# Kernel optimization log

Hardware: AMD Instinct MI355X
Metric: run time of the kernel (lower is better)

The kernel has to match this reference:

```python
import jax, jax.numpy as jnp
import numpy as np

BN_EPS = 1e-5


def _batchnorm(x, gamma, beta):
    # BatchNorm1d in training mode: per-batch mean and biased variance
    mean = jnp.mean(x, axis=0)
    var = jnp.mean((x - mean) ** 2, axis=0)
    return gamma * (x - mean) / jnp.sqrt(var + BN_EPS) + beta


def setup_inputs() -> dict:
    key = jax.random.key(0)
    ks = jax.random.split(key, 8)
    N, D, H, C = 400000, 192, 192, 8
    inputs = jax.random.normal(ks[0], (N, D), dtype=jnp.float32)
    labels = jax.random.randint(ks[1], (N,), 0, C, dtype=jnp.int64)
    s = 0.05
    return {
        "inputs": inputs,
        "labels": labels,
        "W1": jax.random.normal(ks[2], (D, H), dtype=jnp.float32) * s,
        "b1": jnp.zeros((H,), dtype=jnp.float32),
        "g1": jnp.ones((H,), dtype=jnp.float32),
        "be1": jnp.zeros((H,), dtype=jnp.float32),
        "W2": jax.random.normal(ks[3], (H, H), dtype=jnp.float32) * s,
        "b2": jnp.zeros((H,), dtype=jnp.float32),
        "g2": jnp.ones((H,), dtype=jnp.float32),
        "be2": jnp.zeros((H,), dtype=jnp.float32),
        "W3": jax.random.normal(ks[4], (H, C), dtype=jnp.float32) * s,
        "b3": jnp.zeros((C,), dtype=jnp.float32),
    }


def reference(inputs, labels, W1, b1, g1, be1, W2, b2, g2, be2, W3, b3):
    # The per-unique-label mask/concat loop is equivalent to a stable sort by label
    order = jnp.argsort(labels, stable=True)
    fea = inputs[order]              # [N, D]
    domain_ids = labels[order]       # [N]
    # ReverseLayerF is identity in the forward pass
    h = jax.nn.relu(_batchnorm(fea @ W1 + b1, g1, be1))
    h = jax.nn.relu(_batchnorm(h @ W2 + b2, g2, be2))
    pred = jax.nn.sigmoid(h @ W3 + b3)   # [N, C]
    logp = jax.nn.log_softmax(pred, axis=-1)
    loss = -jnp.mean(jnp.take_along_axis(logp, domain_ids[:, None], axis=1))
    return loss
```

## Files before the change

### kernel.cpp

```cpp
#include <hip/hip_runtime.h>

typedef unsigned char u8;
typedef unsigned short u16;
typedef unsigned int u32;
typedef long long i64;
typedef __attribute__((ext_vector_type(2))) float f32x2;
typedef __attribute__((ext_vector_type(4))) float f32x4;

#define NROWS 400000
#define DIM 192
#define GRPB 64
#define GNBLK (NROWS / GRPB)
#define FRPB 128
#define FNBLK (NROWS / FRPB)
#define SLAB 25
#define RBLK (GNBLK / SLAB)
#define PITCH 208
#define BN_EPS 1e-5f

__device__ __forceinline__ u16 f2b(float f) {
  union { float f; u32 u; } v; v.f = f;
  return (u16)((v.u + 0x7fffu + ((v.u >> 16) & 1u)) >> 16);
}

#if __has_builtin(__builtin_amdgcn_cvt_pk_fp8_f32) && __has_builtin(__builtin_amdgcn_cvt_pk_f32_fp8)
#define HW_FP8 1
#endif

__device__ __forceinline__ u32 enc1_fp8(float f) {
  float a = fabsf(f);
  u32 sg = (__float_as_uint(f) >> 24) & 0x80u;
  a = fminf(a, 448.f);
  u32 em;
  if (a >= 0.015625f) {
    u32 b = __float_as_uint(a);
    b += 0x0007FFFFu + ((b >> 20) & 1u);
    em = ((b >> 20) & 0xFFFu) - 960u;
  } else {
    em = (u32)(int)rintf(a * 512.f);
  }
  return sg | em;
}
__device__ __forceinline__ float dec1_fp8(u32 b) {
  u32 em = b & 0x7Fu;
  float vn = __uint_as_float((em + 960u) << 20);
  float vd = (float)em * 0.001953125f;
  float v = (em >= 8u) ? vn : vd;
  return (b & 0x80u) ? -v : v;
}

__device__ __forceinline__ u32 pack4_fp8(float f0, float f1, float f2, float f3) {
#ifdef HW_FP8
  int w = 0;
  w = __builtin_amdgcn_cvt_pk_fp8_f32(f0, f1, w, false);
  w = __builtin_amdgcn_cvt_pk_fp8_f32(f2, f3, w, true);
  return (u32)w;
#else
  return enc1_fp8(f0) | (enc1_fp8(f1) << 8) | (enc1_fp8(f2) << 16) | (enc1_fp8(f3) << 24);
#endif
}

__device__ __forceinline__ void unpack8_fp8(uint2 p, float (&f)[8]) {
#ifdef HW_FP8
  f32x2 v0 = __builtin_amdgcn_cvt_pk_f32_fp8(p.x, false);
  f32x2 v1 = __builtin_amdgcn_cvt_pk_f32_fp8(p.x, true);
  f32x2 v2 = __builtin_amdgcn_cvt_pk_f32_fp8(p.y, false);
  f32x2 v3 = __builtin_amdgcn_cvt_pk_f32_fp8(p.y, true);
  f[0] = v0[0]; f[1] = v0[1]; f[2] = v1[0]; f[3] = v1[1];
  f[4] = v2[0]; f[5] = v2[1]; f[6] = v3[0]; f[7] = v3[1];
#else
#pragma unroll
  for (int i = 0; i < 4; ++i) f[i] = dec1_fp8((p.x >> (8 * i)) & 0xFFu);
#pragma unroll
  for (int i = 0; i < 4; ++i) f[4 + i] = dec1_fp8((p.y >> (8 * i)) & 0xFFu);
#endif
}

__device__ __forceinline__ i64 u2l(uint2 u) {
  union { uint2 u2; i64 l; } c; c.u2 = u; return c.l;
}

__global__ void prep_w(const float* __restrict__ W1, const float* __restrict__ W2,
                       const float* __restrict__ W3, u8* __restrict__ W1q,
                       u8* __restrict__ W2q, u8* __restrict__ W3q) {
  int idx = blockIdx.x * 256 + threadIdx.x;
  if (idx < DIM * DIM) {
    int h = idx / DIM, d = idx % DIM;
    W1q[idx] = (u8)enc1_fp8(W1[d * DIM + h]);
    W2q[idx] = (u8)enc1_fp8(W2[d * DIM + h]);
  } else if (idx < DIM * DIM + 16 * DIM) {
    int j = idx - DIM * DIM;
    int c = j / DIM, k = j % DIM;
    W3q[j] = (c < 8) ? (u8)enc1_fp8(W3[k * 8 + c]) : (u8)0;
  }
}

template <int LAYER>
__global__ __launch_bounds__(256, 4) void gemm_bn(
    const float* __restrict__ Xf, const u8* __restrict__ Yin8,
    u8* __restrict__ Yout8, const u8* __restrict__ Wq,
    const float* __restrict__ bias, const float* __restrict__ scale_in,
    const float* __restrict__ shift_in, float* __restrict__ partials) {
  __shared__ __align__(16) char smem[GRPB * PITCH];
  const int t = threadIdx.x;
  const int bid = blockIdx.x;
  const size_t row0 = (size_t)bid * GRPB;

  if (LAYER == 1) {
    const float4* Xv = (const float4*)(Xf + row0 * DIM);
#pragma unroll
    for (int j = 0; j < 12; ++j) {
      int e = j * 256 + t;
      int r = e / 48, c4 = e % 48;
      float4 v = Xv[e];
      *(u32*)(smem + r * PITCH + c4 * 4) = pack4_fp8(v.x, v.y, v.z, v.w);
    }
  } else {
    const uint2* Yin2 = (const uint2*)(Yin8 + row0 * DIM);
#pragma unroll
    for (int j = 0; j < 6; ++j) {
      int e = j * 256 + t;
      int r = e / 24, c8 = e % 24;
      int cb8 = c8 * 8;
      uint2 p = Yin2[r * 24 + c8];
      float f[8];
      unpack8_fp8(p, f);
      float4 sc0 = *(const float4*)&scale_in[cb8];
      float4 sc1 = *(const float4*)&scale_in[cb8 + 4];
      float4 sh0 = *(const float4*)&shift_in[cb8];
      float4 sh1 = *(const float4*)&shift_in[cb8 + 4];
      float scv[8] = {sc0.x, sc0.y, sc0.z, sc0.w, sc1.x, sc1.y, sc1.z, sc1.w};
      float shv[8] = {sh0.x, sh0.y, sh0.z, sh0.w, sh1.x, sh1.y, sh1.z, sh1.w};
      float h[8];
#pragma unroll
      for (int i = 0; i < 8; ++i) h[i] = fmaxf(f[i] * scv[i] + shv[i], 0.f);
      uint2 o;
      o.x = pack4_fp8(h[0], h[1], h[2], h[3]);
      o.y = pack4_fp8(h[4], h[5], h[6], h[7]);
      *(uint2*)(smem + r * PITCH + cb8) = o;
    }
  }
  __syncthreads();

  const int lane = t & 63, wv = t >> 6;
  const int cb = wv * 48;
  const int lr = lane & 15;
  const int g = lane >> 4;
  const int kg = g * 8;

  f32x4 acc[4][3];
#pragma unroll
  for (int rt = 0; rt < 4; ++rt)
#pragma unroll
    for (int ct = 0; ct < 3; ++ct) acc[rt][ct] = (f32x4){0.f, 0.f, 0.f, 0.f};

#pragma unroll
  for (int ks = 0; ks < 6; ++ks) {
    const int k0 = ks * 32 + kg;
    i64 b0 = u2l(*(const uint2*)(Wq + (size_t)(cb + lr) * DIM + k0));
    i64 b1 = u2l(*(const uint2*)(Wq + (size_t)(cb + 16 + lr) * DIM + k0));
    i64 b2 = u2l(*(const uint2*)(Wq + (size_t)(cb + 32 + lr) * DIM + k0));
#pragma unroll
    for (int rt = 0; rt < 4; ++rt) {
      i64 a = u2l(*(const uint2*)(smem + (rt * 16 + lr) * PITCH + k0));
      acc[rt][0] = __builtin_amdgcn_mfma_f32_16x16x32_fp8_fp8(b0, a, acc[rt][0], 0, 0, 0);
      acc[rt][1] = __builtin_amdgcn_mfma_f32_16x16x32_fp8_fp8(b1, a, acc[rt][1], 0, 0, 0);
      acc[rt][2] = __builtin_amdgcn_mfma_f32_16x16x32_fp8_fp8(b2, a, acc[rt][2], 0, 0, 0);
    }
  }
  __syncthreads();

  float4 bl[3];
#pragma unroll
  for (int ct = 0; ct < 3; ++ct) bl[ct] = *(const float4*)&bias[cb + ct * 16 + g * 4];
  f32x4 s[3], q[3];
#pragma unroll
  for (int ct = 0; ct < 3; ++ct) { s[ct] = (f32x4){0,0,0,0}; q[ct] = (f32x4){0,0,0,0}; }
  u32* lds32 = (u32*)smem;
#pragma unroll
  for (int rt = 0; rt < 4; ++rt) {
    const int row = rt * 16 + lr;
#pragma unroll
    for (int ct = 0; ct < 3; ++ct) {
      f32x4 v = acc[rt][ct];
      float f0 = v[0] + bl[ct].x, f1 = v[1] + bl[ct].y;
      float f2 = v[2] + bl[ct].z, f3 = v[3] + bl[ct].w;
      s[ct][0] += f0; s[ct][1] += f1; s[ct][2] += f2; s[ct][3] += f3;
      q[ct][0] += f0 * f0; q[ct][1] += f1 * f1; q[ct][2] += f2 * f2; q[ct][3] += f3 * f3;
      lds32[row * 52 + wv * 12 + ct * 4 + g] = pack4_fp8(f0, f1, f2, f3);
    }
  }
  __syncthreads();

  uint4* Yo4 = (uint4*)(Yout8 + row0 * DIM);
#pragma unroll
  for (int u = 0; u < 3; ++u) {
    int idx4 = u * 256 + t;
    int row = idx4 / 12, m = idx4 % 12;
    Yo4[idx4] = *(const uint4*)(smem + row * PITCH + m * 16);
  }

#pragma unroll
  for (int ct = 0; ct < 3; ++ct)
#pragma unroll
    for (int off = 1; off <= 8; off <<= 1)
#pragma unroll
      for (int i = 0; i < 4; ++i) {
        s[ct][i] += __shfl_xor(s[ct][i], off);
        q[ct][i] += __shfl_xor(q[ct][i], off);
      }
  if (lr == 0) {
    size_t base = (size_t)bid * 384 + cb + g * 4;
#pragma unroll
    for (int ct = 0; ct < 3; ++ct) {
      *(f32x4*)&partials[base + ct * 16] = s[ct];
      *(f32x4*)&partials[base + ct * 16 + 192] = q[ct];
    }
  }
}

__global__ __launch_bounds__(384) void bn_reduce1(const float* __restrict__ partials,
                                                  float* __restrict__ out2) {
  const int b = blockIdx.x, t = threadIdx.x;
  const float* p = partials + (size_t)b * SLAB * 384;
  float v = 0.f;
#pragma unroll
  for (int r = 0; r < SLAB; ++r) v += p[r * 384 + t];
  out2[b * 384 + t] = v;
}

__global__ __launch_bounds__(384) void bn_fin2(
    const float* __restrict__ out2, const float* __restrict__ g,
    const float* __restrict__ be, float* __restrict__ scale,
    float* __restrict__ shift, float* accum) {
  __shared__ float tot[384];
  const int t = threadIdx.x;
  float v = 0.f;
  for (int b = 0; b < RBLK; ++b) v += out2[b * 384 + t];
  tot[t] = v;
  __syncthreads();
  if (t < 192) {
    float s = tot[t], q = tot[t + 192];
    float mean = s / (float)NROWS;
    float var = q / (float)NROWS - mean * mean;
    float inv = rsqrtf(var + BN_EPS);
    float sc = g[t] * inv;
    scale[t] = sc;
    shift[t] = be[t] - mean * sc;
  }
  if (t == 0) *accum = 0.f;
}

__global__ __launch_bounds__(256, 4) void final_loss(
    const u8* __restrict__ Y2, const int* __restrict__ labels,
    const float* __restrict__ scale2, const float* __restrict__ shift2,
    const u8* __restrict__ W3q, const float* __restrict__ b3, float* accum) {
  __shared__ __align__(16) char smem[FRPB * PITCH];
  __shared__ __align__(16) float sc2[DIM], sh2[DIM];
  __shared__ float red[4];
  const int t = threadIdx.x;
  const size_t row0 = (size_t)blockIdx.x * FRPB;

  const uint4* Yp4 = (const uint4*)(Y2 + row0 * DIM);
#pragma unroll
  for (int j = 0; j < 6; ++j) {
    int idx4 = j * 256 + t;
    int row = idx4 / 12, m = idx4 % 12;
    *(uint4*)(smem + row * PITCH + m * 16) = Yp4[idx4];
  }
  if (t < 48) ((float4*)sc2)[t] = ((const float4*)scale2)[t];
  else if (t < 96) ((float4*)sh2)[t - 48] = ((const float4*)shift2)[t - 48];
  __syncthreads();

  const int lane = t & 63, wv = t >> 6;
  const int lr = lane & 15, g = lane >> 4, kg = g * 8;
  i64 wf[6];
#pragma unroll
  for (int ks = 0; ks < 6; ++ks)
    wf[ks] = u2l(*(const uint2*)(W3q + lr * DIM + ks * 32 + kg));
  const float b3v = (lr < 8) ? b3[lr] : 0.f;

  float contrib = 0.f;
#pragma unroll
  for (int tl = 0; tl < 2; ++tl) {
    const int rbase = wv * 32 + tl * 16;
    f32x4 acc = (f32x4){0.f, 0.f, 0.f, 0.f};
#pragma unroll
    for (int ks = 0; ks < 6; ++ks) {
      const int k0 = ks * 32 + kg;
      uint2 raw = *(const uint2*)(smem + (rbase + lr) * PITCH + k0);
      float f[8];
      unpack8_fp8(raw, f);
      float4 c0 = *(const float4*)&sc2[k0];
      float4 c1 = *(const float4*)&sc2[k0 + 4];
      float4 d0 = *(const float4*)&sh2[k0];
      float4 d1 = *(const float4*)&sh2[k0 + 4];
      float scv[8] = {c0.x, c0.y, c0.z, c0.w, c1.x, c1.y, c1.z, c1.w};
      float shv[8] = {d0.x, d0.y, d0.z, d0.w, d1.x, d1.y, d1.z, d1.w};
      float h[8];
#pragma unroll
      for (int i = 0; i < 8; ++i) h[i] = fmaxf(f[i] * scv[i] + shv[i], 0.f);
      uint2 af;
      af.x = pack4_fp8(h[0], h[1], h[2], h[3]);
      af.y = pack4_fp8(h[4], h[5], h[6], h[7]);
      acc = __builtin_amdgcn_mfma_f32_16x16x32_fp8_fp8(u2l(af), wf[ks], acc, 0, 0, 0);
    }
#pragma unroll
    for (int i = 0; i < 4; ++i) {
      float p = 1.f / (1.f + __expf(-(acc[i] + b3v)));
      float m = p;
      m = fmaxf(m, __shfl_xor(m, 1));
      m = fmaxf(m, __shfl_xor(m, 2));
      m = fmaxf(m, __shfl_xor(m, 4));
      float e = __expf(p - m);
      e += __shfl_xor(e, 1);
      e += __shfl_xor(e, 2);
      e += __shfl_xor(e, 4);
      int lab = labels[row0 + rbase + g * 4 + i];
      if (lr == lab) contrib += m + __logf(e) - p;
    }
  }
#pragma unroll
  for (int off = 1; off < 64; off <<= 1) contrib += __shfl_xor(contrib, off);
  if (lane == 0) red[wv] = contrib;
  __syncthreads();
  if (t == 0) atomicAdd(accum, red[0] + red[1] + red[2] + red[3]);
}

__global__ void finalize(const float* __restrict__ accum, float* __restrict__ out) {
  if (threadIdx.x == 0) out[0] = accum[0] / (float)NROWS;
}

extern "C" void kernel_launch(void* const* d_in, const int* in_sizes, int n_in,
                              void* d_out, int out_size, void* d_ws, size_t ws_size,
                              hipStream_t stream) {
  const float* inputs = (const float*)d_in[0];
  const int* labels   = (const int*)d_in[1];
  const float* W1  = (const float*)d_in[2];
  const float* b1  = (const float*)d_in[3];
  const float* g1  = (const float*)d_in[4];
  const float* be1 = (const float*)d_in[5];
  const float* W2  = (const float*)d_in[6];
  const float* b2  = (const float*)d_in[7];
  const float* g2  = (const float*)d_in[8];
  const float* be2 = (const float*)d_in[9];
  const float* W3  = (const float*)d_in[10];
  const float* b3  = (const float*)d_in[11];
  float* out = (float*)d_out;

  char* ws = (char*)d_ws;
  u8* W1q       = (u8*)(ws + 0);
  u8* W2q       = (u8*)(ws + 40960);
  u8* W3q       = (u8*)(ws + 81920);
  float* scale1 = (float*)(ws + 98304);
  float* shift1 = (float*)(ws + 99072);
  float* scale2 = (float*)(ws + 99840);
  float* shift2 = (float*)(ws + 100608);
  float* accum  = (float*)(ws + 101376);
  float* out2   = (float*)(ws + 102400);
  float* partials = (float*)(ws + 524288);
  u8* Ybuf      = (u8*)(ws + 16777216);

  prep_w<<<300, 256, 0, stream>>>(W1, W2, W3, W1q, W2q, W3q);
  gemm_bn<1><<<GNBLK, 256, 0, stream>>>(inputs, nullptr, Ybuf, W1q, b1, nullptr, nullptr, partials);
  bn_reduce1<<<RBLK, 384, 0, stream>>>(partials, out2);
  bn_fin2<<<1, 384, 0, stream>>>(out2, g1, be1, scale1, shift1, accum);
  gemm_bn<2><<<GNBLK, 256, 0, stream>>>(nullptr, Ybuf, Ybuf, W2q, b2, scale1, shift1, partials);
  bn_reduce1<<<RBLK, 384, 0, stream>>>(partials, out2);
  bn_fin2<<<1, 384, 0, stream>>>(out2, g2, be2, scale2, shift2, accum);
  final_loss<<<FNBLK, 256, 0, stream>>>(Ybuf, labels, scale2, shift2, W3q, b3, accum);
  finalize<<<1, 64, 0, stream>>>(accum, out);
}
```

Before: 231.8 us.

## Persist GEMM blocks with double-buffered LDS prefetch and drop BN-cancelled biases

Turns gemm_bn and final_loss into persistent kernels over a fixed grid of 768 blocks. Each block loads its weight fragments into registers once, then prefetches the next tile into registers and stages it into a second LDS buffer while the current tile is processed. The b1/b2 bias adds are removed because training-mode batchnorm subtracts the batch mean, which cancels them exactly. Other changes: the LDS pitch shrinks to 200 bytes, the BN apply in final_loss moves into the staging step, and prep_w launches fewer blocks. In exchange, register pressure rises and the occupancy bound drops from 4 to 3 blocks per CU.

```diff
diff --git a/kernel.cpp b/kernel.cpp
--- a/kernel.cpp
+++ b/kernel.cpp
@@ -1,7 +1,6 @@
 #include <hip/hip_runtime.h>
 
 typedef unsigned char u8;
-typedef unsigned short u16;
 typedef unsigned int u32;
 typedef long long i64;
 typedef __attribute__((ext_vector_type(2))) float f32x2;
@@ -10,18 +9,15 @@
 #define NROWS 400000
 #define DIM 192
 #define GRPB 64
-#define GNBLK (NROWS / GRPB)
+#define NTILE (NROWS / GRPB)
+#define GGRID 768
 #define FRPB 128
-#define FNBLK (NROWS / FRPB)
+#define FNTILE (NROWS / FRPB)
+#define FGRID 768
 #define SLAB 25
-#define RBLK (GNBLK / SLAB)
-#define PITCH 208
+#define RBLK (NTILE / SLAB)
+#define PITCH 200
 #define BN_EPS 1e-5f
-
-__device__ __forceinline__ u16 f2b(float f) {
-  union { float f; u32 u; } v; v.f = f;
-  return (u16)((v.u + 0x7fffu + ((v.u >> 16) & 1u)) >> 16);
-}
 
 #if __has_builtin(__builtin_amdgcn_cvt_pk_fp8_f32) && __has_builtin(__builtin_amdgcn_cvt_pk_f32_fp8)
 #define HW_FP8 1
@@ -41,13 +37,6 @@
   }
   return sg | em;
 }
-__device__ __forceinline__ float dec1_fp8(u32 b) {
-  u32 em = b & 0x7Fu;
-  float vn = __uint_as_float((em + 960u) << 20);
-  float vd = (float)em * 0.001953125f;
-  float v = (em >= 8u) ? vn : vd;
-  return (b & 0x80u) ? -v : v;
-}
 
 __device__ __forceinline__ u32 pack4_fp8(float f0, float f1, float f2, float f3) {
 #ifdef HW_FP8
@@ -59,6 +48,16 @@
   return enc1_fp8(f0) | (enc1_fp8(f1) << 8) | (enc1_fp8(f2) << 16) | (enc1_fp8(f3) << 24);
 #endif
 }
+
+#ifndef HW_FP8
+__device__ __forceinline__ float dec1_fp8(u32 b) {
+  u32 em = b & 0x7Fu;
+  float vn = __uint_as_float((em + 960u) << 20);
+  float vd = (float)em * 0.001953125f;
+  float v = (em >= 8u) ? vn : vd;
+  return (b & 0x80u) ? -v : v;
+}
+#endif
 
 __device__ __forceinline__ void unpack8_fp8(uint2 p, float (&f)[8]) {
 #ifdef HW_FP8
@@ -96,127 +95,152 @@
 }
 
 template <int LAYER>
-__global__ __launch_bounds__(256, 4) void gemm_bn(
+__global__ __launch_bounds__(256, 3) void gemm_bn(
     const float* __restrict__ Xf, const u8* __restrict__ Yin8,
     u8* __restrict__ Yout8, const u8* __restrict__ Wq,
-    const float* __restrict__ bias, const float* __restrict__ scale_in,
-    const float* __restrict__ shift_in, float* __restrict__ partials) {
-  __shared__ __align__(16) char smem[GRPB * PITCH];
+    const float* __restrict__ scale_in, const float* __restrict__ shift_in,
+    float* __restrict__ partials) {
+  __shared__ __align__(16) char smem[2][GRPB * PITCH];
   const int t = threadIdx.x;
-  const int bid = blockIdx.x;
-  const size_t row0 = (size_t)bid * GRPB;
-
-  if (LAYER == 1) {
-    const float4* Xv = (const float4*)(Xf + row0 * DIM);
-#pragma unroll
-    for (int j = 0; j < 12; ++j) {
-      int e = j * 256 + t;
-      int r = e / 48, c4 = e % 48;
-      float4 v = Xv[e];
-      *(u32*)(smem + r * PITCH + c4 * 4) = pack4_fp8(v.x, v.y, v.z, v.w);
-    }
-  } else {
-    const uint2* Yin2 = (const uint2*)(Yin8 + row0 * DIM);
-#pragma unroll
-    for (int j = 0; j < 6; ++j) {
-      int e = j * 256 + t;
-      int r = e / 24, c8 = e % 24;
-      int cb8 = c8 * 8;
-      uint2 p = Yin2[r * 24 + c8];
-      float f[8];
-      unpack8_fp8(p, f);
-      float4 sc0 = *(const float4*)&scale_in[cb8];
-      float4 sc1 = *(const float4*)&scale_in[cb8 + 4];
-      float4 sh0 = *(const float4*)&shift_in[cb8];
-      float4 sh1 = *(const float4*)&shift_in[cb8 + 4];
-      float scv[8] = {sc0.x, sc0.y, sc0.z, sc0.w, sc1.x, sc1.y, sc1.z, sc1.w};
-      float shv[8] = {sh0.x, sh0.y, sh0.z, sh0.w, sh1.x, sh1.y, sh1.z, sh1.w};
-      float h[8];
-#pragma unroll
-      for (int i = 0; i < 8; ++i) h[i] = fmaxf(f[i] * scv[i] + shv[i], 0.f);
-      uint2 o;
-      o.x = pack4_fp8(h[0], h[1], h[2], h[3]);
-      o.y = pack4_fp8(h[4], h[5], h[6], h[7]);
-      *(uint2*)(smem + r * PITCH + cb8) = o;
-    }
-  }
-  __syncthreads();
-
   const int lane = t & 63, wv = t >> 6;
-  const int cb = wv * 48;
-  const int lr = lane & 15;
-  const int g = lane >> 4;
-  const int kg = g * 8;
-
-  f32x4 acc[4][3];
-#pragma unroll
-  for (int rt = 0; rt < 4; ++rt)
-#pragma unroll
-    for (int ct = 0; ct < 3; ++ct) acc[rt][ct] = (f32x4){0.f, 0.f, 0.f, 0.f};
-
+  const int cb = wv * 48, lr = lane & 15, g = lane >> 4, kg = g * 8;
+
+  i64 wf0[6], wf1[6], wf2[6];
 #pragma unroll
   for (int ks = 0; ks < 6; ++ks) {
     const int k0 = ks * 32 + kg;
-    i64 b0 = u2l(*(const uint2*)(Wq + (size_t)(cb + lr) * DIM + k0));
-    i64 b1 = u2l(*(const uint2*)(Wq + (size_t)(cb + 16 + lr) * DIM + k0));
-    i64 b2 = u2l(*(const uint2*)(Wq + (size_t)(cb + 32 + lr) * DIM + k0));
+    wf0[ks] = u2l(*(const uint2*)(Wq + (size_t)(cb + lr) * DIM + k0));
+    wf1[ks] = u2l(*(const uint2*)(Wq + (size_t)(cb + 16 + lr) * DIM + k0));
+    wf2[ks] = u2l(*(const uint2*)(Wq + (size_t)(cb + 32 + lr) * DIM + k0));
+  }
+
+  float4 xv[12];
+  uint2 yv[6];
+
+#define G_STAGE_LOAD(TILE)                                                   \
+  do {                                                                       \
+    if (LAYER == 1) {                                                        \
+      const float4* Xv = (const float4*)(Xf + (size_t)(TILE) * GRPB * DIM);  \
+      _Pragma("unroll") for (int j = 0; j < 12; ++j) xv[j] = Xv[j * 256 + t];\
+    } else {                                                                 \
+      const uint2* Yv = (const uint2*)(Yin8 + (size_t)(TILE) * GRPB * DIM);  \
+      _Pragma("unroll") for (int j = 0; j < 6; ++j) yv[j] = Yv[j * 256 + t]; \
+    }                                                                        \
+  } while (0)
+
+#define G_STAGE_WRITE(B)                                                     \
+  do {                                                                       \
+    if (LAYER == 1) {                                                        \
+      _Pragma("unroll") for (int j = 0; j < 12; ++j) {                       \
+        int e = j * 256 + t, r = e / 48, c4 = e % 48;                        \
+        *(u32*)(smem[B] + r * PITCH + c4 * 4) =                              \
+            pack4_fp8(xv[j].x, xv[j].y, xv[j].z, xv[j].w);                   \
+      }                                                                      \
+    } else {                                                                 \
+      _Pragma("unroll") for (int j = 0; j < 6; ++j) {                        \
+        int e = j * 256 + t, r = e / 24, cb8 = (e % 24) * 8;                 \
+        float f[8];                                                          \
+        unpack8_fp8(yv[j], f);                                               \
+        float4 sc0 = *(const float4*)&scale_in[cb8];                         \
+        float4 sc1 = *(const float4*)&scale_in[cb8 + 4];                     \
+        float4 sh0 = *(const float4*)&shift_in[cb8];                         \
+        float4 sh1 = *(const float4*)&shift_in[cb8 + 4];                     \
+        float scv[8] = {sc0.x, sc0.y, sc0.z, sc0.w, sc1.x, sc1.y, sc1.z, sc1.w}; \
+        float shv[8] = {sh0.x, sh0.y, sh0.z, sh0.w, sh1.x, sh1.y, sh1.z, sh1.w}; \
+        float h[8];                                                          \
+        _Pragma("unroll") for (int i = 0; i < 8; ++i)                        \
+            h[i] = fmaxf(f[i] * scv[i] + shv[i], 0.f);                       \
+        uint2 o;                                                             \
+        o.x = pack4_fp8(h[0], h[1], h[2], h[3]);                             \
+        o.y = pack4_fp8(h[4], h[5], h[6], h[7]);                             \
+        *(uint2*)(smem[B] + r * PITCH + cb8) = o;                            \
+      }                                                                      \
+    }                                                                        \
+  } while (0)
+
+  int tile = blockIdx.x;
+  G_STAGE_LOAD(tile);
+  G_STAGE_WRITE(0);
+  int p = 0;
+
+  while (true) {
+    const int next = tile + GGRID;
+    const bool more = (next < NTILE);
+    if (more) G_STAGE_LOAD(next);
+    __syncthreads();
+
+    f32x4 acc[4][3];
+#pragma unroll
+    for (int rt = 0; rt < 4; ++rt)
+#pragma unroll
+      for (int ct = 0; ct < 3; ++ct) acc[rt][ct] = (f32x4){0.f, 0.f, 0.f, 0.f};
+
+#pragma unroll
+    for (int ks = 0; ks < 6; ++ks) {
+      const int k0 = ks * 32 + kg;
+#pragma unroll
+      for (int rt = 0; rt < 4; ++rt) {
+        i64 a = u2l(*(const uint2*)(smem[p] + (rt * 16 + lr) * PITCH + k0));
+        acc[rt][0] = __builtin_amdgcn_mfma_f32_16x16x32_fp8_fp8(wf0[ks], a, acc[rt][0], 0, 0, 0);
+        acc[rt][1] = __builtin_amdgcn_mfma_f32_16x16x32_fp8_fp8(wf1[ks], a, acc[rt][1], 0, 0, 0);
+        acc[rt][2] = __builtin_amdgcn_mfma_f32_16x16x32_fp8_fp8(wf2[ks], a, acc[rt][2], 0, 0, 0);
+      }
+    }
+    __syncthreads();
+
+    if (more) G_STAGE_WRITE(p ^ 1);
+
+    f32x4 s[3], q[3];
+#pragma unroll
+    for (int ct = 0; ct < 3; ++ct) { s[ct] = (f32x4){0,0,0,0}; q[ct] = (f32x4){0,0,0,0}; }
+    u32* lds32 = (u32*)smem[p];
 #pragma unroll
     for (int rt = 0; rt < 4; ++rt) {
-      i64 a = u2l(*(const uint2*)(smem + (rt * 16 + lr) * PITCH + k0));
-      acc[rt][0] = __builtin_amdgcn_mfma_f32_16x16x32_fp8_fp8(b0, a, acc[rt][0], 0, 0, 0);
-      acc[rt][1] = __builtin_amdgcn_mfma_f32_16x16x32_fp8_fp8(b1, a, acc[rt][1], 0, 0, 0);
-      acc[rt][2] = __builtin_amdgcn_mfma_f32_16x16x32_fp8_fp8(b2, a, acc[rt][2], 0, 0, 0);
+      const int row = rt * 16 + lr;
+#pragma unroll
+      for (int ct = 0; ct < 3; ++ct) {
+        f32x4 v = acc[rt][ct];
+        s[ct][0] += v[0]; s[ct][1] += v[1]; s[ct][2] += v[2]; s[ct][3] += v[3];
+        q[ct][0] += v[0]*v[0]; q[ct][1] += v[1]*v[1]; q[ct][2] += v[2]*v[2]; q[ct][3] += v[3]*v[3];
+        lds32[row * 50 + wv * 12 + ct * 4 + g] = pack4_fp8(v[0], v[1], v[2], v[3]);
+      }
     }
-  }
-  __syncthreads();
-
-  float4 bl[3];
-#pragma unroll
-  for (int ct = 0; ct < 3; ++ct) bl[ct] = *(const float4*)&bias[cb + ct * 16 + g * 4];
-  f32x4 s[3], q[3];
-#pragma unroll
-  for (int ct = 0; ct < 3; ++ct) { s[ct] = (f32x4){0,0,0,0}; q[ct] = (f32x4){0,0,0,0}; }
-  u32* lds32 = (u32*)smem;
-#pragma unroll
-  for (int rt = 0; rt < 4; ++rt) {
-    const int row = rt * 16 + lr;
-#pragma unroll
-    for (int ct = 0; ct < 3; ++ct) {
-      f32x4 v = acc[rt][ct];
-      float f0 = v[0] + bl[ct].x, f1 = v[1] + bl[ct].y;
-      float f2 = v[2] + bl[ct].z, f3 = v[3] + bl[ct].w;
-      s[ct][0] += f0; s[ct][1] += f1; s[ct][2] += f2; s[ct][3] += f3;
-      q[ct][0] += f0 * f0; q[ct][1] += f1 * f1; q[ct][2] += f2 * f2; q[ct][3] += f3 * f3;
-      lds32[row * 52 + wv * 12 + ct * 4 + g] = pack4_fp8(f0, f1, f2, f3);
+    __syncthreads();
+
+    uint4* Yo4 = (uint4*)(Yout8 + (size_t)tile * GRPB * DIM);
+    const uint2* l2 = (const uint2*)smem[p];
+#pragma unroll
+    for (int u = 0; u < 3; ++u) {
+      int idx4 = u * 256 + t;
+      int row = idx4 / 12, m = idx4 % 12;
+      uint2 a = l2[row * 25 + m * 2];
+      uint2 b = l2[row * 25 + m * 2 + 1];
+      Yo4[idx4] = (uint4){a.x, a.y, b.x, b.y};
     }
-  }
-  __syncthreads();
-
-  uint4* Yo4 = (uint4*)(Yout8 + row0 * DIM);
-#pragma unroll
-  for (int u = 0; u < 3; ++u) {
-    int idx4 = u * 256 + t;
-    int row = idx4 / 12, m = idx4 % 12;
-    Yo4[idx4] = *(const uint4*)(smem + row * PITCH + m * 16);
-  }
-
-#pragma unroll
-  for (int ct = 0; ct < 3; ++ct)
-#pragma unroll
-    for (int off = 1; off <= 8; off <<= 1)
-#pragma unroll
-      for (int i = 0; i < 4; ++i) {
-        s[ct][i] += __shfl_xor(s[ct][i], off);
-        q[ct][i] += __shfl_xor(q[ct][i], off);
+
+#pragma unroll
+    for (int ct = 0; ct < 3; ++ct)
+#pragma unroll
+      for (int off = 1; off <= 8; off <<= 1)
+#pragma unroll
+        for (int i = 0; i < 4; ++i) {
+          s[ct][i] += __shfl_xor(s[ct][i], off);
+          q[ct][i] += __shfl_xor(q[ct][i], off);
+        }
+    if (lr == 0) {
+      size_t base = (size_t)tile * 384 + cb + g * 4;
+#pragma unroll
+      for (int ct = 0; ct < 3; ++ct) {
+        *(f32x4*)&partials[base + ct * 16] = s[ct];
+        *(f32x4*)&partials[base + ct * 16 + 192] = q[ct];
       }
-  if (lr == 0) {
-    size_t base = (size_t)bid * 384 + cb + g * 4;
-#pragma unroll
-    for (int ct = 0; ct < 3; ++ct) {
-      *(f32x4*)&partials[base + ct * 16] = s[ct];
-      *(f32x4*)&partials[base + ct * 16 + 192] = q[ct];
     }
-  }
+    if (!more) break;
+    tile = next;
+    p ^= 1;
+  }
+#undef G_STAGE_LOAD
+#undef G_STAGE_WRITE
 }
 
 __global__ __launch_bounds__(384) void bn_reduce1(const float* __restrict__ partials,
@@ -251,75 +275,103 @@
   if (t == 0) *accum = 0.f;
 }
 
-__global__ __launch_bounds__(256, 4) void final_loss(
+__global__ __launch_bounds__(256, 3) void final_loss(
     const u8* __restrict__ Y2, const int* __restrict__ labels,
     const float* __restrict__ scale2, const float* __restrict__ shift2,
     const u8* __restrict__ W3q, const float* __restrict__ b3, float* accum) {
-  __shared__ __align__(16) char smem[FRPB * PITCH];
-  __shared__ __align__(16) float sc2[DIM], sh2[DIM];
+  __shared__ __align__(16) char smem[2][FRPB * PITCH];
+  __shared__ __align__(16) float sc2s[DIM], sh2s[DIM];
   __shared__ float red[4];
   const int t = threadIdx.x;
-  const size_t row0 = (size_t)blockIdx.x * FRPB;
-
-  const uint4* Yp4 = (const uint4*)(Y2 + row0 * DIM);
-#pragma unroll
-  for (int j = 0; j < 6; ++j) {
-    int idx4 = j * 256 + t;
-    int row = idx4 / 12, m = idx4 % 12;
-    *(uint4*)(smem + row * PITCH + m * 16) = Yp4[idx4];
-  }
-  if (t < 48) ((float4*)sc2)[t] = ((const float4*)scale2)[t];
-  else if (t < 96) ((float4*)sh2)[t - 48] = ((const float4*)shift2)[t - 48];
-  __syncthreads();
-
   const int lane = t & 63, wv = t >> 6;
   const int lr = lane & 15, g = lane >> 4, kg = g * 8;
+
   i64 wf[6];
 #pragma unroll
   for (int ks = 0; ks < 6; ++ks)
     wf[ks] = u2l(*(const uint2*)(W3q + lr * DIM + ks * 32 + kg));
   const float b3v = (lr < 8) ? b3[lr] : 0.f;
-
+  if (t < 48) ((float4*)sc2s)[t] = ((const float4*)scale2)[t];
+  else if (t < 96) ((float4*)sh2s)[t - 48] = ((const float4*)shift2)[t - 48];
+  __syncthreads();
+
+  uint4 fv[6];
+
+#define F_STAGE_LOAD(TILE)                                                   \
+  do {                                                                       \
+    const uint4* Yp4 = (const uint4*)(Y2 + (size_t)(TILE) * FRPB * DIM);     \
+    _Pragma("unroll") for (int j = 0; j < 6; ++j) fv[j] = Yp4[j * 256 + t];  \
+  } while (0)
+
+#define F_STAGE_WRITE(B)                                                     \
+  do {                                                                       \
+    _Pragma("unroll") for (int j = 0; j < 6; ++j) {                          \
+      int idx4 = j * 256 + t, row = idx4 / 12, c0 = (idx4 % 12) * 16;        \
+      uint2 plo = {fv[j].x, fv[j].y}, phi = {fv[j].z, fv[j].w};              \
+      float fa[8], fb[8];                                                    \
+      unpack8_fp8(plo, fa);                                                  \
+      unpack8_fp8(phi, fb);                                                  \
+      float h[16];                                                           \
+      _Pragma("unroll") for (int i = 0; i < 8; ++i) {                        \
+        h[i] = fmaxf(fa[i] * sc2s[c0 + i] + sh2s[c0 + i], 0.f);              \
+        h[8 + i] = fmaxf(fb[i] * sc2s[c0 + 8 + i] + sh2s[c0 + 8 + i], 0.f);  \
+      }                                                                      \
+      uint2 o0 = {pack4_fp8(h[0], h[1], h[2], h[3]),                         \
+                  pack4_fp8(h[4], h[5], h[6], h[7])};                        \
+      uint2 o1 = {pack4_fp8(h[8], h[9], h[10], h[11]),                       \
+                  pack4_fp8(h[12], h[13], h[14], h[15])};                    \
+      *(uint2*)(smem[B] + row * PITCH + c0) = o0;                            \
+      *(uint2*)(smem[B] + row * PITCH + c0 + 8) = o1;                        \
+    }                                                                        \
+  } while (0)
+
+  int tile = blockIdx.x;
+  F_STAGE_LOAD(tile);
+  F_STAGE_WRITE(0);
   float contrib = 0.f;
-#pragma unroll
-  for (int tl = 0; tl < 2; ++tl) {
-    const int rbase = wv * 32 + tl * 16;
-    f32x4 acc = (f32x4){0.f, 0.f, 0.f, 0.f};
-#pragma unroll
-    for (int ks = 0; ks < 6; ++ks) {
-      const int k0 = ks * 32 + kg;
-      uint2 raw = *(const uint2*)(smem + (rbase + lr) * PITCH + k0);
-      float f[8];
-      unpack8_fp8(raw, f);
-      float4 c0 = *(const float4*)&sc2[k0];
-      float4 c1 = *(const float4*)&sc2[k0 + 4];
-      float4 d0 = *(const float4*)&sh2[k0];
-      float4 d1 = *(const float4*)&sh2[k0 + 4];
-      float scv[8] = {c0.x, c0.y, c0.z, c0.w, c1.x, c1.y, c1.z, c1.w};
-      float shv[8] = {d0.x, d0.y, d0.z, d0.w, d1.x, d1.y, d1.z, d1.w};
-      float h[8];
-#pragma unroll
-      for (int i = 0; i < 8; ++i) h[i] = fmaxf(f[i] * scv[i] + shv[i], 0.f);
-      uint2 af;
-      af.x = pack4_fp8(h[0], h[1], h[2], h[3]);
-      af.y = pack4_fp8(h[4], h[5], h[6], h[7]);
-      acc = __builtin_amdgcn_mfma_f32_16x16x32_fp8_fp8(u2l(af), wf[ks], acc, 0, 0, 0);
+  int p = 0;
+
+  while (true) {
+    const int next = tile + FGRID;
+    const bool more = (next < FNTILE);
+    if (more) F_STAGE_LOAD(next);
+    __syncthreads();
+
+    const size_t row0 = (size_t)tile * FRPB;
+#pragma unroll
+    for (int tl = 0; tl < 2; ++tl) {
+      const int rbase = wv * 32 + tl * 16;
+      f32x4 acc = (f32x4){0.f, 0.f, 0.f, 0.f};
+#pragma unroll
+      for (int ks = 0; ks < 6; ++ks) {
+        const int k0 = ks * 32 + kg;
+        i64 a = u2l(*(const uint2*)(smem[p] + (rbase + lr) * PITCH + k0));
+        acc = __builtin_amdgcn_mfma_f32_16x16x32_fp8_fp8(a, wf[ks], acc, 0, 0, 0);
+      }
+#pragma unroll
+      for (int i = 0; i < 4; ++i) {
+        float pv = 1.f / (1.f + __expf(-(acc[i] + b3v)));
+        float m = pv;
+        m = fmaxf(m, __shfl_xor(m, 1));
+        m = fmaxf(m, __shfl_xor(m, 2));
+        m = fmaxf(m, __shfl_xor(m, 4));
+        float e = __expf(pv - m);
+        e += __shfl_xor(e, 1);
+        e += __shfl_xor(e, 2);
+        e += __shfl_xor(e, 4);
+        int lab = labels[row0 + rbase + g * 4 + i];
+        if (lr == lab) contrib += m + __logf(e) - pv;
+      }
     }
-#pragma unroll
-    for (int i = 0; i < 4; ++i) {
-      float p = 1.f / (1.f + __expf(-(acc[i] + b3v)));
-      float m = p;
-      m = fmaxf(m, __shfl_xor(m, 1));
-      m = fmaxf(m, __shfl_xor(m, 2));
-      m = fmaxf(m, __shfl_xor(m, 4));
-      float e = __expf(p - m);
-      e += __shfl_xor(e, 1);
-      e += __shfl_xor(e, 2);
-      e += __shfl_xor(e, 4);
-      int lab = labels[row0 + rbase + g * 4 + i];
-      if (lr == lab) contrib += m + __logf(e) - p;
-    }
-  }
+    __syncthreads();
+    if (!more) break;
+    F_STAGE_WRITE(p ^ 1);
+    tile = next;
+    p ^= 1;
+  }
+#undef F_STAGE_LOAD
+#undef F_STAGE_WRITE
+
 #pragma unroll
   for (int off = 1; off < 64; off <<= 1) contrib += __shfl_xor(contrib, off);
   if (lane == 0) red[wv] = contrib;
@@ -337,11 +389,9 @@
   const float* inputs = (const float*)d_in[0];
   const int* labels   = (const int*)d_in[1];
   const float* W1  = (const float*)d_in[2];
-  const float* b1  = (const float*)d_in[3];
   const float* g1  = (const float*)d_in[4];
   const float* be1 = (const float*)d_in[5];
   const float* W2  = (const float*)d_in[6];
-  const float* b2  = (const float*)d_in[7];
   const float* g2  = (const float*)d_in[8];
   const float* be2 = (const float*)d_in[9];
   const float* W3  = (const float*)d_in[10];
@@ -361,13 +411,13 @@
   float* partials = (float*)(ws + 524288);
   u8* Ybuf      = (u8*)(ws + 16777216);
 
-  prep_w<<<300, 256, 0, stream>>>(W1, W2, W3, W1q, W2q, W3q);
-  gemm_bn<1><<<GNBLK, 256, 0, stream>>>(inputs, nullptr, Ybuf, W1q, b1, nullptr, nullptr, partials);
+  prep_w<<<156, 256, 0, stream>>>(W1, W2, W3, W1q, W2q, W3q);
+  gemm_bn<1><<<GGRID, 256, 0, stream>>>(inputs, nullptr, Ybuf, W1q, nullptr, nullptr, partials);
   bn_reduce1<<<RBLK, 384, 0, stream>>>(partials, out2);
   bn_fin2<<<1, 384, 0, stream>>>(out2, g1, be1, scale1, shift1, accum);
-  gemm_bn<2><<<GNBLK, 256, 0, stream>>>(nullptr, Ybuf, Ybuf, W2q, b2, scale1, shift1, partials);
+  gemm_bn<2><<<GGRID, 256, 0, stream>>>(nullptr, Ybuf, Ybuf, W2q, scale1, shift1, partials);
   bn_reduce1<<<RBLK, 384, 0, stream>>>(partials, out2);
   bn_fin2<<<1, 384, 0, stream>>>(out2, g2, be2, scale2, shift2, accum);
-  final_loss<<<FNBLK, 256, 0, stream>>>(Ybuf, labels, scale2, shift2, W3q, b3, accum);
+  final_loss<<<FGRID, 256, 0, stream>>>(Ybuf, labels, scale2, shift2, W3q, b3, accum);
   finalize<<<1, 64, 0, stream>>>(accum, out);
 }
```

After: 330.0 us (median of 2 runs). +42.4%, slower.

## Make GEMM+BN kernels persistent with register-resident weights and prefetched tiles

Applied to the files above, without the earlier changes.

The two GEMM+BN layers now run as a persistent grid of 1024 blocks over 32-row tiles. Each block keeps its fp8 weight fragments in registers and prefetches the next tile's input from global memory while it computes the current tile's MFMAs, with separate LDS buffers for input and output. The linear biases are dropped because the following batch norm subtracts the mean and cancels them. The final loss kernel applies BN and ReLU once while staging rows into LDS, instead of inside the MFMA k-loop. This trades more registers and a lower grid size for hiding memory latency and less redundant per-tile work.

```diff
diff --git a/kernel.cpp b/kernel.cpp
--- a/kernel.cpp
+++ b/kernel.cpp
@@ -1,7 +1,6 @@
 #include <hip/hip_runtime.h>
 
 typedef unsigned char u8;
-typedef unsigned short u16;
 typedef unsigned int u32;
 typedef long long i64;
 typedef __attribute__((ext_vector_type(2))) float f32x2;
@@ -9,19 +8,16 @@
 
 #define NROWS 400000
 #define DIM 192
-#define GRPB 64
-#define GNBLK (NROWS / GRPB)
+#define GRPB 32
+#define GNTILE (NROWS / GRPB)
+#define GGRID 1024
 #define FRPB 128
-#define FNBLK (NROWS / FRPB)
-#define SLAB 25
-#define RBLK (GNBLK / SLAB)
-#define PITCH 208
+#define FNTILE (NROWS / FRPB)
+#define SLAB 50
+#define RBLK (GNTILE / SLAB)
+#define GPITCH 200
+#define FPITCH 208
 #define BN_EPS 1e-5f
-
-__device__ __forceinline__ u16 f2b(float f) {
-  union { float f; u32 u; } v; v.f = f;
-  return (u16)((v.u + 0x7fffu + ((v.u >> 16) & 1u)) >> 16);
-}
 
 #if __has_builtin(__builtin_amdgcn_cvt_pk_fp8_f32) && __has_builtin(__builtin_amdgcn_cvt_pk_f32_fp8)
 #define HW_FP8 1
@@ -41,13 +37,6 @@
   }
   return sg | em;
 }
-__device__ __forceinline__ float dec1_fp8(u32 b) {
-  u32 em = b & 0x7Fu;
-  float vn = __uint_as_float((em + 960u) << 20);
-  float vd = (float)em * 0.001953125f;
-  float v = (em >= 8u) ? vn : vd;
-  return (b & 0x80u) ? -v : v;
-}
 
 __device__ __forceinline__ u32 pack4_fp8(float f0, float f1, float f2, float f3) {
 #ifdef HW_FP8
@@ -59,6 +48,16 @@
   return enc1_fp8(f0) | (enc1_fp8(f1) << 8) | (enc1_fp8(f2) << 16) | (enc1_fp8(f3) << 24);
 #endif
 }
+
+#ifndef HW_FP8
+__device__ __forceinline__ float dec1_fp8(u32 b) {
+  u32 em = b & 0x7Fu;
+  float vn = __uint_as_float((em + 960u) << 20);
+  float vd = (float)em * 0.001953125f;
+  float v = (em >= 8u) ? vn : vd;
+  return (b & 0x80u) ? -v : v;
+}
+#endif
 
 __device__ __forceinline__ void unpack8_fp8(uint2 p, float (&f)[8]) {
 #ifdef HW_FP8
@@ -99,123 +98,149 @@
 __global__ __launch_bounds__(256, 4) void gemm_bn(
     const float* __restrict__ Xf, const u8* __restrict__ Yin8,
     u8* __restrict__ Yout8, const u8* __restrict__ Wq,
-    const float* __restrict__ bias, const float* __restrict__ scale_in,
-    const float* __restrict__ shift_in, float* __restrict__ partials) {
-  __shared__ __align__(16) char smem[GRPB * PITCH];
+    const float* __restrict__ scale_in, const float* __restrict__ shift_in,
+    float* __restrict__ partials) {
+  __shared__ __align__(16) char sin[GRPB * GPITCH];
+  __shared__ __align__(16) u32 sout[GRPB * 50];
+  __shared__ float scs[DIM], shs[DIM];
   const int t = threadIdx.x;
-  const int bid = blockIdx.x;
-  const size_t row0 = (size_t)bid * GRPB;
-
-  if (LAYER == 1) {
-    const float4* Xv = (const float4*)(Xf + row0 * DIM);
-#pragma unroll
-    for (int j = 0; j < 12; ++j) {
-      int e = j * 256 + t;
-      int r = e / 48, c4 = e % 48;
-      float4 v = Xv[e];
-      *(u32*)(smem + r * PITCH + c4 * 4) = pack4_fp8(v.x, v.y, v.z, v.w);
-    }
-  } else {
-    const uint2* Yin2 = (const uint2*)(Yin8 + row0 * DIM);
-#pragma unroll
-    for (int j = 0; j < 6; ++j) {
-      int e = j * 256 + t;
-      int r = e / 24, c8 = e % 24;
-      int cb8 = c8 * 8;
-      uint2 p = Yin2[r * 24 + c8];
-      float f[8];
-      unpack8_fp8(p, f);
-      float4 sc0 = *(const float4*)&scale_in[cb8];
-      float4 sc1 = *(const float4*)&scale_in[cb8 + 4];
-      float4 sh0 = *(const float4*)&shift_in[cb8];
-      float4 sh1 = *(const float4*)&shift_in[cb8 + 4];
-      float scv[8] = {sc0.x, sc0.y, sc0.z, sc0.w, sc1.x, sc1.y, sc1.z, sc1.w};
-      float shv[8] = {sh0.x, sh0.y, sh0.z, sh0.w, sh1.x, sh1.y, sh1.z, sh1.w};
-      float h[8];
-#pragma unroll
-      for (int i = 0; i < 8; ++i) h[i] = fmaxf(f[i] * scv[i] + shv[i], 0.f);
-      uint2 o;
-      o.x = pack4_fp8(h[0], h[1], h[2], h[3]);
-      o.y = pack4_fp8(h[4], h[5], h[6], h[7]);
-      *(uint2*)(smem + r * PITCH + cb8) = o;
-    }
-  }
-  __syncthreads();
-
   const int lane = t & 63, wv = t >> 6;
-  const int cb = wv * 48;
-  const int lr = lane & 15;
-  const int g = lane >> 4;
-  const int kg = g * 8;
-
-  f32x4 acc[4][3];
-#pragma unroll
-  for (int rt = 0; rt < 4; ++rt)
-#pragma unroll
-    for (int ct = 0; ct < 3; ++ct) acc[rt][ct] = (f32x4){0.f, 0.f, 0.f, 0.f};
-
+  const int cb = wv * 48, lr = lane & 15, g = lane >> 4, kg = g * 8;
+
+  i64 wf0[6], wf1[6], wf2[6];
 #pragma unroll
   for (int ks = 0; ks < 6; ++ks) {
     const int k0 = ks * 32 + kg;
-    i64 b0 = u2l(*(const uint2*)(Wq + (size_t)(cb + lr) * DIM + k0));
-    i64 b1 = u2l(*(const uint2*)(Wq + (size_t)(cb + 16 + lr) * DIM + k0));
-    i64 b2 = u2l(*(const uint2*)(Wq + (size_t)(cb + 32 + lr) * DIM + k0));
-#pragma unroll
-    for (int rt = 0; rt < 4; ++rt) {
-      i64 a = u2l(*(const uint2*)(smem + (rt * 16 + lr) * PITCH + k0));
-      acc[rt][0] = __builtin_amdgcn_mfma_f32_16x16x32_fp8_fp8(b0, a, acc[rt][0], 0, 0, 0);
-      acc[rt][1] = __builtin_amdgcn_mfma_f32_16x16x32_fp8_fp8(b1, a, acc[rt][1], 0, 0, 0);
-      acc[rt][2] = __builtin_amdgcn_mfma_f32_16x16x32_fp8_fp8(b2, a, acc[rt][2], 0, 0, 0);
-    }
-  }
-  __syncthreads();
-
-  float4 bl[3];
-#pragma unroll
-  for (int ct = 0; ct < 3; ++ct) bl[ct] = *(const float4*)&bias[cb + ct * 16 + g * 4];
-  f32x4 s[3], q[3];
-#pragma unroll
-  for (int ct = 0; ct < 3; ++ct) { s[ct] = (f32x4){0,0,0,0}; q[ct] = (f32x4){0,0,0,0}; }
-  u32* lds32 = (u32*)smem;
-#pragma unroll
-  for (int rt = 0; rt < 4; ++rt) {
-    const int row = rt * 16 + lr;
-#pragma unroll
-    for (int ct = 0; ct < 3; ++ct) {
-      f32x4 v = acc[rt][ct];
-      float f0 = v[0] + bl[ct].x, f1 = v[1] + bl[ct].y;
-      float f2 = v[2] + bl[ct].z, f3 = v[3] + bl[ct].w;
-      s[ct][0] += f0; s[ct][1] += f1; s[ct][2] += f2; s[ct][3] += f3;
-      q[ct][0] += f0 * f0; q[ct][1] += f1 * f1; q[ct][2] += f2 * f2; q[ct][3] += f3 * f3;
-      lds32[row * 52 + wv * 12 + ct * 4 + g] = pack4_fp8(f0, f1, f2, f3);
-    }
-  }
-  __syncthreads();
-
-  uint4* Yo4 = (uint4*)(Yout8 + row0 * DIM);
-#pragma unroll
-  for (int u = 0; u < 3; ++u) {
-    int idx4 = u * 256 + t;
-    int row = idx4 / 12, m = idx4 % 12;
-    Yo4[idx4] = *(const uint4*)(smem + row * PITCH + m * 16);
-  }
-
-#pragma unroll
-  for (int ct = 0; ct < 3; ++ct)
-#pragma unroll
-    for (int off = 1; off <= 8; off <<= 1)
-#pragma unroll
-      for (int i = 0; i < 4; ++i) {
-        s[ct][i] += __shfl_xor(s[ct][i], off);
-        q[ct][i] += __shfl_xor(q[ct][i], off);
-      }
-  if (lr == 0) {
-    size_t base = (size_t)bid * 384 + cb + g * 4;
-#pragma unroll
-    for (int ct = 0; ct < 3; ++ct) {
-      *(f32x4*)&partials[base + ct * 16] = s[ct];
-      *(f32x4*)&partials[base + ct * 16 + 192] = q[ct];
-    }
+    wf0[ks] = u2l(*(const uint2*)(Wq + (size_t)(cb + lr) * DIM + k0));
+    wf1[ks] = u2l(*(const uint2*)(Wq + (size_t)(cb + 16 + lr) * DIM + k0));
+    wf2[ks] = u2l(*(const uint2*)(Wq + (size_t)(cb + 32 + lr) * DIM + k0));
+  }
+  if (LAYER == 2) {
+    if (t < 48) *(float4*)&scs[t * 4] = ((const float4*)scale_in)[t];
+    else if (t < 96) *(float4*)&shs[(t - 48) * 4] = ((const float4*)shift_in)[t - 48];
+  }
+
+  float4 xv[6];
+  uint2 yv[3];
+
+  auto LOADS = [&](int tl) {
+    if (LAYER == 1) {
+      const float4* Xv = (const float4*)Xf + (size_t)tl * (GRPB * DIM / 4);
+#pragma unroll
+      for (int j = 0; j < 6; ++j) xv[j] = Xv[j * 256 + t];
+    } else {
+      const uint2* Yv = (const uint2*)(Yin8 + (size_t)tl * GRPB * DIM);
+#pragma unroll
+      for (int j = 0; j < 3; ++j) yv[j] = Yv[j * 256 + t];
+    }
+  };
+  auto SWRITE = [&]() {
+    if (LAYER == 1) {
+#pragma unroll
+      for (int j = 0; j < 6; ++j) {
+        int e = j * 256 + t, r = e / 48, c4 = e % 48;
+        *(u32*)(sin + r * GPITCH + c4 * 4) =
+            pack4_fp8(xv[j].x, xv[j].y, xv[j].z, xv[j].w);
+      }
+    } else {
+#pragma unroll
+      for (int j = 0; j < 3; ++j) {
+        int e = j * 256 + t, r = e / 24, cb8 = (e % 24) * 8;
+        float f[8];
+        unpack8_fp8(yv[j], f);
+        float h[8];
+#pragma unroll
+        for (int i = 0; i < 8; ++i)
+          h[i] = fmaxf(f[i] * scs[cb8 + i] + shs[cb8 + i], 0.f);
+        uint2 o;
+        o.x = pack4_fp8(h[0], h[1], h[2], h[3]);
+        o.y = pack4_fp8(h[4], h[5], h[6], h[7]);
+        *(uint2*)(sin + r * GPITCH + cb8) = o;
+      }
+    }
+  };
+
+  int tile = blockIdx.x;
+  LOADS(tile);
+  asm volatile("s_waitcnt lgkmcnt(0)" ::: "memory");
+  __builtin_amdgcn_s_barrier();
+  SWRITE();
+  asm volatile("s_waitcnt lgkmcnt(0)" ::: "memory");
+  __builtin_amdgcn_s_barrier();
+
+  while (true) {
+    const int next = tile + GGRID;
+    const bool more = next < GNTILE;
+    if (more) LOADS(next);
+
+    f32x4 acc[2][3];
+#pragma unroll
+    for (int rt = 0; rt < 2; ++rt)
+#pragma unroll
+      for (int ct = 0; ct < 3; ++ct) acc[rt][ct] = (f32x4){0.f, 0.f, 0.f, 0.f};
+
+#pragma unroll
+    for (int ks = 0; ks < 6; ++ks) {
+      const int k0 = ks * 32 + kg;
+#pragma unroll
+      for (int rt = 0; rt < 2; ++rt) {
+        i64 a = u2l(*(const uint2*)(sin + (rt * 16 + lr) * GPITCH + k0));
+        acc[rt][0] = __builtin_amdgcn_mfma_f32_16x16x32_fp8_fp8(wf0[ks], a, acc[rt][0], 0, 0, 0);
+        acc[rt][1] = __builtin_amdgcn_mfma_f32_16x16x32_fp8_fp8(wf1[ks], a, acc[rt][1], 0, 0, 0);
+        acc[rt][2] = __builtin_amdgcn_mfma_f32_16x16x32_fp8_fp8(wf2[ks], a, acc[rt][2], 0, 0, 0);
+      }
+    }
+
+    f32x4 s[3], q[3];
+#pragma unroll
+    for (int ct = 0; ct < 3; ++ct) { s[ct] = (f32x4){0,0,0,0}; q[ct] = (f32x4){0,0,0,0}; }
+#pragma unroll
+    for (int rt = 0; rt < 2; ++rt) {
+      const int row = rt * 16 + lr;
+#pragma unroll
+      for (int ct = 0; ct < 3; ++ct) {
+        f32x4 v = acc[rt][ct];
+        s[ct][0] += v[0]; s[ct][1] += v[1]; s[ct][2] += v[2]; s[ct][3] += v[3];
+        q[ct][0] += v[0]*v[0]; q[ct][1] += v[1]*v[1]; q[ct][2] += v[2]*v[2]; q[ct][3] += v[3]*v[3];
+        sout[row * 50 + wv * 12 + ct * 4 + g] = pack4_fp8(v[0], v[1], v[2], v[3]);
+      }
+    }
+    asm volatile("s_waitcnt lgkmcnt(0)" ::: "memory");
+    __builtin_amdgcn_s_barrier();
+
+    if (more) SWRITE();
+
+    {
+      u8* yb = Yout8 + (size_t)tile * GRPB * DIM;
+#pragma unroll
+      for (int k = 0; k < 3; ++k) {
+        int idx = k * 256 + t;
+        int row = idx / 24, m = idx % 24;
+        uint2 v = *(const uint2*)&sout[row * 50 + 2 * m];
+        *(uint2*)(yb + (size_t)idx * 8) = v;
+      }
+    }
+#pragma unroll
+    for (int ct = 0; ct < 3; ++ct)
+#pragma unroll
+      for (int off = 1; off <= 8; off <<= 1)
+#pragma unroll
+        for (int i = 0; i < 4; ++i) {
+          s[ct][i] += __shfl_xor(s[ct][i], off);
+          q[ct][i] += __shfl_xor(q[ct][i], off);
+        }
+    if (lr == 0) {
+      size_t base = (size_t)tile * 384 + cb + g * 4;
+#pragma unroll
+      for (int ct = 0; ct < 3; ++ct) {
+        *(f32x4*)&partials[base + ct * 16] = s[ct];
+        *(f32x4*)&partials[base + ct * 16 + 192] = q[ct];
+      }
+    }
+    asm volatile("s_waitcnt lgkmcnt(0)" ::: "memory");
+    __builtin_amdgcn_s_barrier();
+    if (!more) break;
+    tile = next;
   }
 }
 
@@ -255,23 +280,39 @@
     const u8* __restrict__ Y2, const int* __restrict__ labels,
     const float* __restrict__ scale2, const float* __restrict__ shift2,
     const u8* __restrict__ W3q, const float* __restrict__ b3, float* accum) {
-  __shared__ __align__(16) char smem[FRPB * PITCH];
+  __shared__ __align__(16) char smem[FRPB * FPITCH];
   __shared__ __align__(16) float sc2[DIM], sh2[DIM];
   __shared__ float red[4];
   const int t = threadIdx.x;
   const size_t row0 = (size_t)blockIdx.x * FRPB;
 
-  const uint4* Yp4 = (const uint4*)(Y2 + row0 * DIM);
-#pragma unroll
-  for (int j = 0; j < 6; ++j) {
-    int idx4 = j * 256 + t;
-    int row = idx4 / 12, m = idx4 % 12;
-    *(uint4*)(smem + row * PITCH + m * 16) = Yp4[idx4];
-  }
   if (t < 48) ((float4*)sc2)[t] = ((const float4*)scale2)[t];
   else if (t < 96) ((float4*)sh2)[t - 48] = ((const float4*)shift2)[t - 48];
   __syncthreads();
 
+  const uint4* Yp4 = (const uint4*)(Y2 + row0 * DIM);
+#pragma unroll
+  for (int j = 0; j < 6; ++j) {
+    int idx4 = j * 256 + t;
+    int row = idx4 / 12, c0 = (idx4 % 12) * 16;
+    uint4 p = Yp4[idx4];
+    uint2 plo = {p.x, p.y}, phi = {p.z, p.w};
+    float fa[8], fb[8];
+    unpack8_fp8(plo, fa);
+    unpack8_fp8(phi, fb);
+    float h[16];
+#pragma unroll
+    for (int i = 0; i < 8; ++i) {
+      h[i] = fmaxf(fa[i] * sc2[c0 + i] + sh2[c0 + i], 0.f);
+      h[8 + i] = fmaxf(fb[i] * sc2[c0 + 8 + i] + sh2[c0 + 8 + i], 0.f);
+    }
+    uint2 o0 = {pack4_fp8(h[0], h[1], h[2], h[3]), pack4_fp8(h[4], h[5], h[6], h[7])};
+    uint2 o1 = {pack4_fp8(h[8], h[9], h[10], h[11]), pack4_fp8(h[12], h[13], h[14], h[15])};
+    *(uint2*)(smem + row * FPITCH + c0) = o0;
+    *(uint2*)(smem + row * FPITCH + c0 + 8) = o1;
+  }
+  __syncthreads();
+
   const int lane = t & 63, wv = t >> 6;
   const int lr = lane & 15, g = lane >> 4, kg = g * 8;
   i64 wf[6];
@@ -288,36 +329,22 @@
 #pragma unroll
     for (int ks = 0; ks < 6; ++ks) {
       const int k0 = ks * 32 + kg;
-      uint2 raw = *(const uint2*)(smem + (rbase + lr) * PITCH + k0);
-      float f[8];
-      unpack8_fp8(raw, f);
-      float4 c0 = *(const float4*)&sc2[k0];
-      float4 c1 = *(const float4*)&sc2[k0 + 4];
-      float4 d0 = *(const float4*)&sh2[k0];
-      float4 d1 = *(const float4*)&sh2[k0 + 4];
-      float scv[8] = {c0.x, c0.y, c0.z, c0.w, c1.x, c1.y, c1.z, c1.w};
-      float shv[8] = {d0.x, d0.y, d0.z, d0.w, d1.x, d1.y, d1.z, d1.w};
-      float h[8];
-#pragma unroll
-      for (int i = 0; i < 8; ++i) h[i] = fmaxf(f[i] * scv[i] + shv[i], 0.f);
-      uint2 af;
-      af.x = pack4_fp8(h[0], h[1], h[2], h[3]);
-      af.y = pack4_fp8(h[4], h[5], h[6], h[7]);
-      acc = __builtin_amdgcn_mfma_f32_16x16x32_fp8_fp8(u2l(af), wf[ks], acc, 0, 0, 0);
+      i64 a = u2l(*(const uint2*)(smem + (rbase + lr) * FPITCH + k0));
+      acc = __builtin_amdgcn_mfma_f32_16x16x32_fp8_fp8(a, wf[ks], acc, 0, 0, 0);
     }
 #pragma unroll
     for (int i = 0; i < 4; ++i) {
-      float p = 1.f / (1.f + __expf(-(acc[i] + b3v)));
-      float m = p;
+      float pv = 1.f / (1.f + __expf(-(acc[i] + b3v)));
+      float m = pv;
       m = fmaxf(m, __shfl_xor(m, 1));
       m = fmaxf(m, __shfl_xor(m, 2));
       m = fmaxf(m, __shfl_xor(m, 4));
-      float e = __expf(p - m);
+      float e = __expf(pv - m);
       e += __shfl_xor(e, 1);
       e += __shfl_xor(e, 2);
       e += __shfl_xor(e, 4);
       int lab = labels[row0 + rbase + g * 4 + i];
-      if (lr == lab) contrib += m + __logf(e) - p;
+      if (lr == lab) contrib += m + __logf(e) - pv;
     }
   }
 #pragma unroll
@@ -337,11 +364,9 @@
   const float* inputs = (const float*)d_in[0];
   const int* labels   = (const int*)d_in[1];
   const float* W1  = (const float*)d_in[2];
-  const float* b1  = (const float*)d_in[3];
   const float* g1  = (const float*)d_in[4];
   const float* be1 = (const float*)d_in[5];
   const float* W2  = (const float*)d_in[6];
-  const float* b2  = (const float*)d_in[7];
   const float* g2  = (const float*)d_in[8];
   const float* be2 = (const float*)d_in[9];
   const float* W3  = (const float*)d_in[10];
@@ -359,15 +384,15 @@
   float* accum  = (float*)(ws + 101376);
   float* out2   = (float*)(ws + 102400);
   float* partials = (float*)(ws + 524288);
-  u8* Ybuf      = (u8*)(ws + 16777216);
-
-  prep_w<<<300, 256, 0, stream>>>(W1, W2, W3, W1q, W2q, W3q);
-  gemm_bn<1><<<GNBLK, 256, 0, stream>>>(inputs, nullptr, Ybuf, W1q, b1, nullptr, nullptr, partials);
+  u8* Ybuf      = (u8*)(ws + 20971520);
+
+  prep_w<<<156, 256, 0, stream>>>(W1, W2, W3, W1q, W2q, W3q);
+  gemm_bn<1><<<GGRID, 256, 0, stream>>>(inputs, nullptr, Ybuf, W1q, nullptr, nullptr, partials);
   bn_reduce1<<<RBLK, 384, 0, stream>>>(partials, out2);
   bn_fin2<<<1, 384, 0, stream>>>(out2, g1, be1, scale1, shift1, accum);
-  gemm_bn<2><<<GNBLK, 256, 0, stream>>>(nullptr, Ybuf, Ybuf, W2q, b2, scale1, shift1, partials);
+  gemm_bn<2><<<GGRID, 256, 0, stream>>>(nullptr, Ybuf, Ybuf, W2q, scale1, shift1, partials);
   bn_reduce1<<<RBLK, 384, 0, stream>>>(partials, out2);
   bn_fin2<<<1, 384, 0, stream>>>(out2, g2, be2, scale2, shift2, accum);
-  final_loss<<<FNBLK, 256, 0, stream>>>(Ybuf, labels, scale2, shift2, W3q, b3, accum);
+  final_loss<<<FNTILE, 256, 0, stream>>>(Ybuf, labels, scale2, shift2, W3q, b3, accum);
   finalize<<<1, 64, 0, stream>>>(accum, out);
 }
```

Result: slower. 263.9 us (+13.8%).
